# Optimization experiments

Hardware: AMD Instinct MI355X
Metric: run time of the kernel (lower is better)

The kernel has to match this reference:

```python
import jax, jax.numpy as jnp
import numpy as np
from math import log

T, B, IN, H1, H2, OUT = 128, 256, 1024, 2048, 2048, 512
DT, INIT_TAU, MIN_TAU, THRESH, VREST = 0.01, 0.5, 0.1, 1.0, 0.0
SLOPE = 25.0  # snntorch surrogate.fast_sigmoid default slope

@jax.custom_vjp
def spike_fn(x):
    # Heaviside forward; fast-sigmoid surrogate backward
    return (x > 0).astype(x.dtype)

def _spike_fwd(x):
    return spike_fn(x), x

def _spike_bwd(x, g):
    return (g / (SLOPE * jnp.abs(x) + 1.0) ** 2,)

spike_fn.defvjp(_spike_fwd, _spike_bwd)

def setup_inputs() -> dict:
    key = jax.random.key(0)
    ks = jax.random.split(key, 7)
    init_w = -log(1.0 / (INIT_TAU - MIN_TAU) - 1.0)
    def lin(k, fan_in, fan_out):
        bound = 1.0 / np.sqrt(fan_in)
        kw, kb = jax.random.split(k)
        W = jax.random.uniform(kw, (fan_out, fan_in), jnp.float32, -bound, bound)
        b = jax.random.uniform(kb, (fan_out,), jnp.float32, -bound, bound)
        return W, b
    W1, b1 = lin(ks[0], IN, H1)
    W2, b2 = lin(ks[1], H1, H2)
    W3, b3 = lin(ks[2], H2, OUT)
    s = (jax.random.uniform(ks[3], (T, B, IN), jnp.float32) < 0.2).astype(jnp.float32)
    return {
        "s": s,
        "W1": W1, "b1": b1, "wt1": jnp.full((H1,), init_w, jnp.float32),
        "W2": W2, "b2": b2, "wt2": jnp.full((H2,), init_w, jnp.float32),
        "W3": W3, "b3": b3, "wt3": jnp.full((OUT,), init_w, jnp.float32),
    }

def _lif(v, cur, w_tau):
    tau = MIN_TAU + jax.nn.sigmoid(w_tau)
    v = v + (DT / tau) * (-(v - VREST) + cur)  # r = 1.0
    spike = spike_fn(v - THRESH)
    v_post = v * (1.0 - spike)  # zero reset
    return v_post, spike, v  # v is pre-reset membrane (v_tmp)

def reference(s, W1, b1, wt1, W2, b2, wt2, W3, b3, wt3):
    v0 = (jnp.zeros((B, H1), s.dtype), jnp.zeros((B, H2), s.dtype), jnp.zeros((B, OUT), s.dtype))
    def step(carry, st):
        v1, v2, v3 = carry
        v1, s1, _ = _lif(v1, st @ W1.T + b1, wt1)
        v2, s2, _ = _lif(v2, s1 @ W2.T + b2, wt2)
        v3, s3, vtmp = _lif(v3, s2 @ W3.T + b3, wt3)
        return (v1, v2, v3), (s3, vtmp)
    _, (out_s, out_v) = jax.lax.scan(step, v0, s)
    return out_s, out_v
```

## Files before the change

kernel.cpp:

```cpp
#include <hip/hip_runtime.h>
#include <hip/hip_bf16.h>
#include <cstdint>
#include <cstddef>

#define T_STEPS 128
#define BATCH   256
#define IN_F    1024
#define H1_F    2048
#define H2_F    2048
#define OUT_F   512
#define M_TOT   (T_STEPS * BATCH)

#define W1_SCALE 4064.0f
#define W1_INV   (1.0f / 4064.0f)

#define S_F4_BLOCKS 8192
#define W_F4_BLOCKS 512

typedef __attribute__((ext_vector_type(4))) int   int4v;
typedef __attribute__((ext_vector_type(8))) unsigned short ushort8;
typedef unsigned long long ull;

__device__ __forceinline__ void load16_to_lds(const void* g, void* l) {
  __builtin_amdgcn_global_load_lds(
      (const __attribute__((address_space(1))) void*)g,
      (__attribute__((address_space(3))) void*)l, 16, 0, 0);
}

__device__ __forceinline__ unsigned short f2bf(float x) {
  __hip_bfloat16 h = __float2bfloat16(x);
  return *reinterpret_cast<unsigned short*>(&h);
}

__device__ __forceinline__ float bf2f(unsigned short u) {
  unsigned int w = ((unsigned int)u) << 16;
  return *reinterpret_cast<float*>(&w);
}

__device__ __forceinline__ float lif_k(float w) {
  float tau = 0.1f + 1.0f / (1.0f + expf(-w));
  return 0.01f / tau;
}

__global__ __launch_bounds__(256) void cvt_both(
    const float4* __restrict__ s_in, unsigned int* __restrict__ s_out,
    const float4* __restrict__ w_in, unsigned int* __restrict__ w_out) {
  const int tid = threadIdx.x, lane = tid & 63, wv = tid >> 6;
  const int bid = blockIdx.x;
  const bool is_s = bid < S_F4_BLOCKS;
  const float4* in;
  unsigned int* out;
  size_t base;
  if (is_s) {
    in = s_in; out = s_out;
    base = (size_t)bid * 1024 + wv * 256 + lane;
  } else {
    in = w_in; out = w_out;
    base = (size_t)(bid - S_F4_BLOCKS) * 1024 + wv * 256 + lane;
  }
#pragma unroll
  for (int q = 0; q < 4; ++q) {
    float4 v = in[base + q * 64];
    unsigned int p;
    if (is_s) {
      p = (v.x > 0.5f ? 1u : 0u) | (v.y > 0.5f ? 0x100u : 0u) |
          (v.z > 0.5f ? 0x10000u : 0u) | (v.w > 0.5f ? 0x1000000u : 0u);
    } else {
      int c0 = __float2int_rn(v.x * W1_SCALE), c1 = __float2int_rn(v.y * W1_SCALE);
      int c2 = __float2int_rn(v.z * W1_SCALE), c3 = __float2int_rn(v.w * W1_SCALE);
      p = (c0 & 0xff) | ((c1 & 0xff) << 8) | ((c2 & 0xff) << 16) | ((c3 & 0xff) << 24);
    }
    out[base + q * 64] = p;
  }
}

union SMem {
  struct { uint4 lA[2][2048]; uint4 lB[2][2048]; } st;
  unsigned short tile[2][256][136];
};

__global__ __launch_bounds__(512, 2) void gemm_scan(
    const int8_t* __restrict__ A, const int8_t* __restrict__ B,
    const float* __restrict__ b1, const float* __restrict__ wt1,
    ull* __restrict__ mask1) {
  __shared__ SMem sm;
  const int tid = threadIdx.x, lane = tid & 63, wv = tid >> 6;
  const int mk = lane & 15, grp = lane >> 4;
  const int wr = wv >> 2, wc = wv & 3;

  const int id = blockIdx.x;
  const int x = id & 7, j = id >> 3;
  const int mt = x * 16 + (j >> 3);
  const int nt = j & 7;
  const int b0 = mt * 2;
  const int n0 = nt * 256;

  const int8_t* gA[4]; const int8_t* gB[4]; int slot[4];
#pragma unroll
  for (int u = 0; u < 4; ++u) {
    const int s = tid + u * 512;
    const int r = s >> 3;
    const int csw = ((s & 7) ^ (r & 7)) * 16;
    slot[u] = s;
    gA[u] = A + (size_t)((r & 127) * BATCH + b0 + (r >> 7)) * IN_F + csw;
    gB[u] = B + (size_t)(n0 + r) * IN_F + csw;
  }

  int4v acc[8][4] = {};

#pragma unroll
  for (int u = 0; u < 4; ++u) {
    load16_to_lds(gA[u], &sm.st.lA[0][slot[u]]);
    load16_to_lds(gB[u], &sm.st.lB[0][slot[u]]);
  }

#pragma unroll 2
  for (int t = 0; t < 8; ++t) {
    const int cur = t & 1;
    const int kt1 = (t + 1) * 128;
    if (t < 7) {
      load16_to_lds(gA[0] + kt1, &sm.st.lA[cur ^ 1][slot[0]]);
      load16_to_lds(gB[0] + kt1, &sm.st.lB[cur ^ 1][slot[0]]);
      asm volatile("s_waitcnt vmcnt(2)" ::: "memory");
    } else {
      asm volatile("s_waitcnt vmcnt(0)" ::: "memory");
    }
    __builtin_amdgcn_sched_barrier(0);
    __builtin_amdgcn_s_barrier();
    __builtin_amdgcn_sched_barrier(0);

    int4v bfr[4];
#pragma unroll
    for (int p = 0; p < 4; ++p) {
      const int ks = p >> 1, mh = p & 1;
      const int kb = ks * 4 + grp;
      int4v af[4];
      if (mh == 0) {
#pragma unroll
        for (int f = 0; f < 4; ++f) {
          const int n = wc * 64 + f * 16 + mk;
          bfr[f] = *(const int4v*)&sm.st.lB[cur][n * 8 + (kb ^ (n & 7))];
        }
      }
#pragma unroll
      for (int f = 0; f < 4; ++f) {
        const int m = wr * 128 + (mh * 4 + f) * 16 + mk;
        af[f] = *(const int4v*)&sm.st.lA[cur][m * 8 + (kb ^ (m & 7))];
      }
      if (p > 0 && t < 7) {
        load16_to_lds(gA[p] + kt1, &sm.st.lA[cur ^ 1][slot[p]]);
        load16_to_lds(gB[p] + kt1, &sm.st.lB[cur ^ 1][slot[p]]);
      }
      __builtin_amdgcn_sched_barrier(0);
      __builtin_amdgcn_s_barrier();
      __builtin_amdgcn_sched_barrier(0);
      __builtin_amdgcn_s_setprio(1);
#pragma unroll
      for (int i = 0; i < 4; ++i)
#pragma unroll
        for (int jj = 0; jj < 4; ++jj)
          acc[mh * 4 + i][jj] = __builtin_amdgcn_mfma_i32_16x16x64_i8(
              af[i], bfr[jj], acc[mh * 4 + i][jj], 0, 0, 0);
      __builtin_amdgcn_s_setprio(0);
      __builtin_amdgcn_sched_barrier(0);
      __builtin_amdgcn_s_barrier();
      __builtin_amdgcn_sched_barrier(0);
    }
  }

#pragma unroll
  for (int j = 0; j < 4; ++j) {
    const int h = wc * 64 + j * 16 + mk;
#pragma unroll
    for (int i = 0; i < 8; ++i) {
      const int t0 = i * 16 + grp * 4;
      uint2 pk;
      pk.x = ((unsigned int)f2bf((float)acc[i][j][1] * W1_INV) << 16)
           | f2bf((float)acc[i][j][0] * W1_INV);
      pk.y = ((unsigned int)f2bf((float)acc[i][j][3] * W1_INV) << 16)
           | f2bf((float)acc[i][j][2] * W1_INV);
      *(uint2*)&sm.tile[wr][h][t0] = pk;
    }
  }
  __syncthreads();

  {
    const int bl = wv >> 2;
    const int hw = wv & 3;
    const int h  = hw * 64 + lane;
    const int hg = n0 + h;
    const int b  = b0 + bl;
    const float bias = b1[hg];
    const float k    = lif_k(wt1[hg]);
    const size_t wbase = (size_t)(n0 >> 6) + hw;
    float v = 0.0f;
    for (int t8 = 0; t8 < T_STEPS; t8 += 8) {
      ushort8 pk = *(const ushort8*)&sm.tile[bl][h][t8];
#pragma unroll
      for (int u = 0; u < 8; ++u) {
        v = fmaf(k, (bf2f(pk[u]) + bias) - v, v);
        bool sp = v > 1.0f;
        ull bm = __ballot(sp);
        if (lane == 0)
          mask1[((size_t)(t8 + u) * BATCH + b) * (H1_F / 64) + wbase] = bm;
        if (sp) v = 0.0f;
      }
    }
  }
}

__global__ __launch_bounds__(1024) void layer23_kernel(
    const ull* __restrict__ mask1,
    const float* __restrict__ W2, const float* __restrict__ b2, const float* __restrict__ wt2,
    const float* __restrict__ W3, const float* __restrict__ b3, const float* __restrict__ wt3,
    float* __restrict__ out_s, float* __restrict__ out_v) {
  __shared__ ull m1all[T_STEPS * 32];
  __shared__ ull m2sh[2][32];
  const int tid = threadIdx.x, b = blockIdx.x;
  const int lane = tid & 63, wv = tid >> 6;

  const float bias2a = b2[tid], bias2b = b2[tid + 1024];
  const float k2a = lif_k(wt2[tid]), k2b = lif_k(wt2[tid + 1024]);
  const float* W2a = W2 + (size_t)tid * H1_F;
  const float* W2b = W2 + (size_t)(tid + 1024) * H1_F;
  float v2a = 0.0f, v2b = 0.0f;

  float bias3 = 0.0f, k3 = 0.0f, v3 = 0.0f;
  const float* W3r = W3;
  if (wv < 8) {
    bias3 = b3[tid];
    k3 = lif_k(wt3[tid]);
    W3r = W3 + (size_t)tid * H2_F;
  }

#pragma unroll
  for (int u = 0; u < 4; ++u) {
    int idx = tid + u * 1024;
    m1all[idx] = mask1[((size_t)(idx >> 5) * BATCH + b) * 32 + (idx & 31)];
  }
  __syncthreads();

  for (int t = 0; t < T_STEPS; ++t) {
    ull wrd = (lane < 32) ? m1all[t * 32 + lane] : 0ull;

    float cura = bias2a, curb = bias2b;
    if (__ballot(wrd != 0ull)) {
      for (int wi = 0; wi < 32; ++wi) {
        ull m = __shfl(wrd, wi, 64);
        while (m) {
          int bit = __ffsll(m) - 1;
          m &= m - 1;
          int idx = wi * 64 + bit;
          cura += W2a[idx];
          curb += W2b[idx];
        }
      }
    }
    v2a = fmaf(k2a, cura - v2a, v2a);
    v2b = fmaf(k2b, curb - v2b, v2b);
    bool spa = v2a > 1.0f, spb = v2b > 1.0f;
    ull sa = __ballot(spa);
    ull sb = __ballot(spb);
    if (lane == 0) { m2sh[t & 1][wv] = sa; m2sh[t & 1][16 + wv] = sb; }
    if (spa) v2a = 0.0f;
    if (spb) v2b = 0.0f;
    __syncthreads();

    if (wv < 8) {
      ull w3m = (lane < 32) ? m2sh[t & 1][lane] : 0ull;
      float cur3 = bias3;
      if (__ballot(w3m != 0ull)) {
        for (int wi = 0; wi < 32; ++wi) {
          ull m = __shfl(w3m, wi, 64);
          while (m) {
            int bit = __ffsll(m) - 1;
            m &= m - 1;
            cur3 += W3r[wi * 64 + bit];
          }
        }
      }
      float vp = fmaf(k3, cur3 - v3, v3);
      bool sp = vp > 1.0f;
      size_t idx = (size_t)(t * BATCH + b) * OUT_F + tid;
      out_s[idx] = sp ? 1.0f : 0.0f;
      out_v[idx] = vp;
      v3 = sp ? 0.0f : vp;
    }
  }
}

extern "C" void kernel_launch(void* const* d_in, const int* in_sizes, int n_in,
                              void* d_out, int out_size, void* d_ws, size_t ws_size,
                              hipStream_t stream) {
  const float* s   = (const float*)d_in[0];
  const float* W1  = (const float*)d_in[1];
  const float* b1  = (const float*)d_in[2];
  const float* wt1 = (const float*)d_in[3];
  const float* W2  = (const float*)d_in[4];
  const float* b2  = (const float*)d_in[5];
  const float* wt2 = (const float*)d_in[6];
  const float* W3  = (const float*)d_in[7];
  const float* b3  = (const float*)d_in[8];
  const float* wt3 = (const float*)d_in[9];

  char* wsb = (char*)d_ws;
  const size_t MASK_BYTES = (size_t)T_STEPS * BATCH * (H1_F / 64) * 8;
  const size_t S_ELEMS  = (size_t)M_TOT * IN_F;
  ull* mask1 = (ull*)wsb;
  int8_t* s_i8  = (int8_t*)(wsb + MASK_BYTES);
  int8_t* W1_i8 = s_i8 + S_ELEMS;
  (void)ws_size;

  float* outs = (float*)d_out;
  float* outv = outs + (size_t)T_STEPS * BATCH * OUT_F;

  cvt_both<<<S_F4_BLOCKS + W_F4_BLOCKS, 256, 0, stream>>>(
      (const float4*)s, (unsigned int*)s_i8, (const float4*)W1, (unsigned int*)W1_i8);

  gemm_scan<<<(BATCH / 2) * (H1_F / 256), 512, 0, stream>>>(s_i8, W1_i8, b1, wt1, mask1);

  layer23_kernel<<<BATCH, 1024, 0, stream>>>(mask1, W2, b2, wt2, W3, b3, wt3, outs, outv);
}
```

Baseline: 378.1 us.

## Transpose W2/W3 so sparse spike gathers read coalesced rows

Adds a tiled LDS transpose kernel that writes W2 and W3 transposed into workspace memory, reusing the area that held the int8 inputs after the layer-1 GEMM is done. In the layer-2/3 kernel every thread in a wavefront gathers the same input index, so reads along the transposed layout become contiguous across lanes and coalesce, where before each lane hit a different row with a large stride. The cost is one extra kernel launch and about 20 MB of transpose traffic per call. Workspace aliasing relies on the GEMM finishing before the transpose runs on the same stream.

```diff
diff --git a/kernel.cpp b/kernel.cpp
--- a/kernel.cpp
+++ b/kernel.cpp
@@ -74,6 +74,35 @@
   }
 }
 
+__global__ __launch_bounds__(256) void transpose_w(
+    const float* __restrict__ W2, const float* __restrict__ W3,
+    float* __restrict__ W2T, float* __restrict__ W3T) {
+  __shared__ float tl[64][65];
+  int bid = blockIdx.x;
+  const float* src; float* dst; int R, C, tr, tc;
+  if (bid < 1024) {
+    src = W2; dst = W2T; R = 2048; C = 2048;
+    tr = (bid >> 5) * 64; tc = (bid & 31) * 64;
+  } else {
+    bid -= 1024;
+    src = W3; dst = W3T; R = 512; C = 2048;
+    tr = (bid >> 5) * 64; tc = (bid & 31) * 64;
+  }
+  const int t = threadIdx.x;
+  const int c = t & 63, r0 = t >> 6;
+#pragma unroll
+  for (int i = 0; i < 16; ++i) {
+    const int r = r0 + i * 4;
+    tl[r][c] = src[(size_t)(tr + r) * C + tc + c];
+  }
+  __syncthreads();
+#pragma unroll
+  for (int i = 0; i < 16; ++i) {
+    const int r = r0 + i * 4;
+    dst[(size_t)(tc + r) * R + tr + c] = tl[c][r];
+  }
+}
+
 union SMem {
   struct { uint4 lA[2][2048]; uint4 lB[2][2048]; } st;
   unsigned short tile[2][256][136];
@@ -211,8 +240,8 @@
 
 __global__ __launch_bounds__(1024) void layer23_kernel(
     const ull* __restrict__ mask1,
-    const float* __restrict__ W2, const float* __restrict__ b2, const float* __restrict__ wt2,
-    const float* __restrict__ W3, const float* __restrict__ b3, const float* __restrict__ wt3,
+    const float* __restrict__ W2T, const float* __restrict__ b2, const float* __restrict__ wt2,
+    const float* __restrict__ W3T, const float* __restrict__ b3, const float* __restrict__ wt3,
     float* __restrict__ out_s, float* __restrict__ out_v) {
   __shared__ ull m1all[T_STEPS * 32];
   __shared__ ull m2sh[2][32];
@@ -221,16 +250,16 @@
 
   const float bias2a = b2[tid], bias2b = b2[tid + 1024];
   const float k2a = lif_k(wt2[tid]), k2b = lif_k(wt2[tid + 1024]);
-  const float* W2a = W2 + (size_t)tid * H1_F;
-  const float* W2b = W2 + (size_t)(tid + 1024) * H1_F;
+  const float* W2a = W2T + tid;
+  const float* W2b = W2T + tid + 1024;
   float v2a = 0.0f, v2b = 0.0f;
 
   float bias3 = 0.0f, k3 = 0.0f, v3 = 0.0f;
-  const float* W3r = W3;
+  const float* W3r = W3T;
   if (wv < 8) {
     bias3 = b3[tid];
     k3 = lif_k(wt3[tid]);
-    W3r = W3 + (size_t)tid * H2_F;
+    W3r = W3T + tid;
   }
 
 #pragma unroll
@@ -250,9 +279,9 @@
         while (m) {
           int bit = __ffsll(m) - 1;
           m &= m - 1;
-          int idx = wi * 64 + bit;
-          cura += W2a[idx];
-          curb += W2b[idx];
+          size_t off = (size_t)(wi * 64 + bit) * H2_F;
+          cura += W2a[off];
+          curb += W2b[off];
         }
       }
     }
@@ -275,7 +304,7 @@
           while (m) {
             int bit = __ffsll(m) - 1;
             m &= m - 1;
-            cur3 += W3r[wi * 64 + bit];
+            cur3 += W3r[(size_t)(wi * 64 + bit) * OUT_F];
           }
         }
       }
@@ -309,6 +338,8 @@
   ull* mask1 = (ull*)wsb;
   int8_t* s_i8  = (int8_t*)(wsb + MASK_BYTES);
   int8_t* W1_i8 = s_i8 + S_ELEMS;
+  float* W2T = (float*)(wsb + MASK_BYTES);
+  float* W3T = W2T + (size_t)H1_F * H2_F;
   (void)ws_size;
 
   float* outs = (float*)d_out;
@@ -319,5 +350,7 @@
 
   gemm_scan<<<(BATCH / 2) * (H1_F / 256), 512, 0, stream>>>(s_i8, W1_i8, b1, wt1, mask1);
 
-  layer23_kernel<<<BATCH, 1024, 0, stream>>>(mask1, W2, b2, wt2, W3, b3, wt3, outs, outv);
-}
+  transpose_w<<<1024 + 256, 256, 0, stream>>>(W2, W3, W2T, W3T);
+
+  layer23_kernel<<<BATCH, 1024, 0, stream>>>(mask1, W2T, b2, wt2, W3T, b3, wt3, outs, outv);
+}
```

New measurement: 388.5 us. 1.03x slower.
